# Optimization experiments

Measured on AMD Instinct MI355X. Metric: run time of the kernel, lower is better.

The kernel has to match this reference:

```python
import jax, jax.numpy as jnp
import numpy as np

B, H, E, D = 16384, 1024, 64, 128  # batch, hidden, nb_entities, wh_units==we_units


def setup_inputs() -> dict:
    key = jax.random.key(0)
    k0, k1, k2 = jax.random.split(key, 3)
    hidden_state = jax.random.normal(k0, (B, H), dtype=jnp.float32)
    # Wh: Dense(wh_units) acting on H -> D
    Wh_w = jax.random.normal(k1, (H, D), dtype=jnp.float32) * 0.02
    Wh_b = jnp.zeros((D,), dtype=jnp.float32)
    # We: nb_entities separate Dense(we_units), stacked into one [E, D, D] tensor
    We_w = jax.random.normal(k2, (E, D, D), dtype=jnp.float32) * 0.02
    We_b = jnp.zeros((E, D), dtype=jnp.float32)
    return {"hidden_state": hidden_state, "Wh_w": Wh_w, "Wh_b": Wh_b,
            "We_w": We_w, "We_b": We_b}


def reference(hidden_state, Wh_w, Wh_b, We_w, We_b):
    # reduced_dimentionality = Wh(hidden_state)            [B, D]
    r = hidden_state @ Wh_w + Wh_b
    # per-entity Dense loop + concat + transpose == one batched GEMM -> [B, E, D]
    logits = jnp.einsum('bk,ekd->bed', r, We_w) + We_b[None, :, :]
    outputs = jax.nn.softmax(logits, axis=-1)               # [B, E, D]
    # second pass: We[i] applied to outputs[:, i, :]       [B, E, D]
    vt = jnp.einsum('bek,ekd->bed', outputs, We_w) + We_b[None, :, :]
    # transpose to [B, D, E] then reduce_sum over E == sum over entity axis
    result = vt.sum(axis=1)                                 # [B, D]
    return (outputs, result)
```

## Files before the change

kernel.cpp:

```cpp
#include <hip/hip_runtime.h>
#include <hip/hip_bf16.h>

typedef __attribute__((ext_vector_type(8))) short short8;
typedef __attribute__((ext_vector_type(4))) float f32x4;
typedef __attribute__((ext_vector_type(4))) unsigned int uint4v;
typedef __attribute__((ext_vector_type(2))) unsigned int uint2v;

#define NB 16384
#define NH 1024
#define NE 64
#define ND 128
#define BR 32
#define GRP 8

static __device__ __forceinline__ unsigned short f2b(float x) {
  unsigned int u = __builtin_bit_cast(unsigned int, x);
  unsigned int r = (u + 0x7fffu + ((u >> 16) & 1u)) >> 16;
  return (unsigned short)r;
}
static __device__ __forceinline__ float b2f_lo(unsigned int u) {
  return __builtin_bit_cast(float, u << 16);
}
static __device__ __forceinline__ float b2f_hi(unsigned int u) {
  return __builtin_bit_cast(float, u & 0xffff0000u);
}

static __device__ __forceinline__ void bar_sync() {
  __builtin_amdgcn_sched_barrier(0);
  asm volatile("s_waitcnt lgkmcnt(0)" ::: "memory");
  __builtin_amdgcn_sched_barrier(0);
  __builtin_amdgcn_s_barrier();
  __builtin_amdgcn_sched_barrier(0);
}

static __device__ __forceinline__ int swz(int row, int col) {
  return (row << 7) + ((((col >> 3) ^ (row & 15)) << 3) | (col & 7));
}
static __device__ __forceinline__ int pswz(int row, int eg, int col) {
  return ((row * GRP + eg) << 7) + ((((col >> 3) ^ (row & 15)) << 3) | (col & 7));
}

__global__ __launch_bounds__(256, 1) void k0_prep(
    const float* __restrict__ Wh_w, const float* __restrict__ We_w,
    const float* __restrict__ We_b,
    unsigned short* __restrict__ WeT, unsigned short* __restrict__ WhT,
    float* __restrict__ bsum)
{
  __shared__ float tile[32][33];
  const int bid = blockIdx.x, t = threadIdx.x;
  const int i = t >> 5, j = t & 31;
  if (bid < 1024) {
    const int e = bid >> 4, tr = (bid >> 2) & 3, tc = bid & 3;
    const float* src = We_w + (size_t)e * 16384;
#pragma unroll
    for (int k = 0; k < 4; ++k)
      tile[i + 8 * k][j] = src[(size_t)(tr * 32 + i + 8 * k) * 128 + tc * 32 + j];
    __syncthreads();
    unsigned short* dst = WeT + (size_t)e * 16384;
#pragma unroll
    for (int k = 0; k < 4; ++k) {
      int row = i + 8 * k;
      dst[(size_t)(tc * 32 + row) * 128 + tr * 32 + j] = f2b(tile[j][row]);
    }
  } else if (bid < 1152) {
    const int tb = bid - 1024, tr = tb >> 2, tc = tb & 3;
#pragma unroll
    for (int k = 0; k < 4; ++k)
      tile[i + 8 * k][j] = Wh_w[(size_t)(tr * 32 + i + 8 * k) * 128 + tc * 32 + j];
    __syncthreads();
#pragma unroll
    for (int k = 0; k < 4; ++k) {
      int row = i + 8 * k;
      WhT[(size_t)(tc * 32 + row) * 1024 + tr * 32 + j] = f2b(tile[j][row]);
    }
  } else {
    if (t < 128) {
      float s = 0.f;
      for (int e = 0; e < 64; ++e) s += We_b[e * 128 + t];
      bsum[t] = s;
    }
  }
}

__global__ __launch_bounds__(256, 2) void k1_rgemm(
    const float* __restrict__ hidden, const unsigned short* __restrict__ WhT,
    const float* __restrict__ Wh_b, unsigned short* __restrict__ r_g)
{
  const int t = threadIdx.x;
  const int w = t >> 6, l = t & 63, c = l & 15, g = l >> 4;
  const int bg = w & 1, dh = w >> 1;
  const int b = blockIdx.x * 32 + 16 * bg + c;
  const float* hrow = hidden + (size_t)b * NH;
  f32x4 acc[4];
#pragma unroll
  for (int mf = 0; mf < 4; ++mf) acc[mf] = (f32x4){0.f, 0.f, 0.f, 0.f};
#pragma unroll 2
  for (int ks = 0; ks < 32; ++ks) {
    const int k0 = 8 * g + 32 * ks;
    f32x4 h0 = *(const f32x4*)(hrow + k0);
    f32x4 h1 = *(const f32x4*)(hrow + k0 + 4);
    short8 bf;
    bf[0] = (short)f2b(h0[0]); bf[1] = (short)f2b(h0[1]);
    bf[2] = (short)f2b(h0[2]); bf[3] = (short)f2b(h0[3]);
    bf[4] = (short)f2b(h1[0]); bf[5] = (short)f2b(h1[1]);
    bf[6] = (short)f2b(h1[2]); bf[7] = (short)f2b(h1[3]);
#pragma unroll
    for (int mf = 0; mf < 4; ++mf) {
      short8 af = *(const short8*)(WhT + (size_t)(64 * dh + 16 * mf + c) * NH + k0);
      acc[mf] = __builtin_amdgcn_mfma_f32_16x16x32_bf16(af, bf, acc[mf], 0, 0, 0);
    }
  }
#pragma unroll
  for (int mf = 0; mf < 4; ++mf) {
    const int d0 = 64 * dh + 16 * mf + 4 * g;
    f32x4 bias = *(const f32x4*)(Wh_b + d0);
    f32x4 v = acc[mf] + bias;
    unsigned int lo = (unsigned)f2b(v[0]) | ((unsigned)f2b(v[1]) << 16);
    unsigned int hi = (unsigned)f2b(v[2]) | ((unsigned)f2b(v[3]) << 16);
    uint2v pk = {lo, hi};
    *(uint2v*)(r_g + (size_t)b * ND + d0) = pk;
  }
}

struct SmemK2 {
  union {
    unsigned short Pst[BR * GRP * 128];
    float obuf[BR * 128];
  };
  unsigned short r_lds[BR * 128];
  float sms[4][BR];
};

static __device__ __forceinline__ void load_we_frags(
    short8 (&f)[2][4], f32x4 (&bias)[2],
    const unsigned short* __restrict__ WeT, const float* __restrict__ We_b,
    int e, int w, int c, int g)
{
  const unsigned short* base = WeT + (size_t)e * (ND * ND);
#pragma unroll
  for (int mf = 0; mf < 2; ++mf) {
    const unsigned short* rowp = base + (size_t)(16 * (2 * w + mf) + c) * ND + 8 * g;
#pragma unroll
    for (int ks = 0; ks < 4; ++ks)
      f[mf][ks] = *(const short8*)(rowp + 32 * ks);
    bias[mf] = *(const f32x4*)(We_b + e * ND + 32 * w + 16 * mf + 4 * g);
  }
}

static __device__ __forceinline__ void entity_body(
    int eg, int en, int w, int c, int g,
    short8 (&cur)[2][4], short8 (&nxt)[2][4],
    f32x4 (&bcur)[2], f32x4 (&bnxt)[2], f32x4 (&acc2)[2][2],
    const unsigned short* __restrict__ WeT, const float* __restrict__ We_b,
    SmemK2& sm)
{
  f32x4 acc1[2][2];
#pragma unroll
  for (int mf = 0; mf < 2; ++mf)
#pragma unroll
    for (int nf = 0; nf < 2; ++nf) acc1[mf][nf] = (f32x4){0.f, 0.f, 0.f, 0.f};
#pragma unroll
  for (int ks = 0; ks < 4; ++ks) {
    short8 b1[2];
#pragma unroll
    for (int nf = 0; nf < 2; ++nf)
      b1[nf] = *(const short8*)(&sm.r_lds[swz(16 * nf + c, 8 * g + 32 * ks)]);
#pragma unroll
    for (int mf = 0; mf < 2; ++mf)
#pragma unroll
      for (int nf = 0; nf < 2; ++nf)
        acc1[mf][nf] = __builtin_amdgcn_mfma_f32_16x16x32_bf16(
            cur[mf][ks], b1[nf], acc1[mf][nf], 0, 0, 0);
  }
  load_we_frags(nxt, bnxt, WeT, We_b, en, w, c, g);

#pragma unroll
  for (int mf = 0; mf < 2; ++mf)
#pragma unroll
    for (int nf = 0; nf < 2; ++nf) acc1[mf][nf] += bcur[mf];
  float s[2] = {0.f, 0.f};
#pragma unroll
  for (int nf = 0; nf < 2; ++nf) {
#pragma unroll
    for (int mf = 0; mf < 2; ++mf)
#pragma unroll
      for (int r = 0; r < 4; ++r) {
        float p = __expf(acc1[mf][nf][r]);
        acc1[mf][nf][r] = p;
        s[nf] += p;
      }
    s[nf] += __shfl_xor(s[nf], 16);
    s[nf] += __shfl_xor(s[nf], 32);
  }
  if (g == 0) {
#pragma unroll
    for (int nf = 0; nf < 2; ++nf) sm.sms[w][16 * nf + c] = s[nf];
  }
  bar_sync();
  float inv[2];
#pragma unroll
  for (int nf = 0; nf < 2; ++nf) {
    int b = 16 * nf + c;
    inv[nf] = 1.f / (sm.sms[0][b] + sm.sms[1][b] + sm.sms[2][b] + sm.sms[3][b]);
  }
#pragma unroll
  for (int mf = 0; mf < 2; ++mf)
#pragma unroll
    for (int nf = 0; nf < 2; ++nf) {
      f32x4 p = acc1[mf][nf] * inv[nf];
      unsigned int lo = (unsigned)f2b(p[0]) | ((unsigned)f2b(p[1]) << 16);
      unsigned int hi = (unsigned)f2b(p[2]) | ((unsigned)f2b(p[3]) << 16);
      uint2v pk = {lo, hi};
      *(uint2v*)(&sm.Pst[pswz(16 * nf + c, eg, 32 * w + 16 * mf + 4 * g)]) = pk;
    }
  bar_sync();

#pragma unroll
  for (int ks = 0; ks < 4; ++ks) {
    short8 a2[2];
#pragma unroll
    for (int mf2 = 0; mf2 < 2; ++mf2)
      a2[mf2] = *(const short8*)(&sm.Pst[pswz(16 * mf2 + c, eg, 8 * g + 32 * ks)]);
#pragma unroll
    for (int mf2 = 0; mf2 < 2; ++mf2)
#pragma unroll
      for (int n = 0; n < 2; ++n)
        acc2[mf2][n] = __builtin_amdgcn_mfma_f32_16x16x32_bf16(
            a2[mf2], cur[n][ks], acc2[mf2][n], 0, 0, 0);
  }
}

__global__ __launch_bounds__(256, 2) void k2_main(
    const unsigned short* __restrict__ r_g, const unsigned short* __restrict__ WeT,
    const float* __restrict__ We_b, const float* __restrict__ bsum,
    float* __restrict__ outP, float* __restrict__ outR)
{
  __shared__ SmemK2 sm;
  const int t = threadIdx.x;
  const int w = t >> 6, l = t & 63, c = l & 15, g = l >> 4;
  const int lb = (blockIdx.x & 7) * 64 + (blockIdx.x >> 3);
  const int brow0 = lb * BR;
  const int e0 = (((lb >> 6) + lb) & 7) << 3;

  for (int i = t; i < BR * 16; i += 256) {
    int row = i >> 4, ch = i & 15;
    uint4v v = *(const uint4v*)(r_g + (size_t)(brow0 + row) * ND + ch * 8);
    *(uint4v*)(&sm.r_lds[swz(row, ch * 8)]) = v;
  }
  const float bs0 = bsum[32 * w + c];
  const float bs1 = bsum[32 * w + 16 + c];

  f32x4 acc2[2][2];
#pragma unroll
  for (int i = 0; i < 2; ++i)
#pragma unroll
    for (int j = 0; j < 2; ++j) acc2[i][j] = (f32x4){0.f, 0.f, 0.f, 0.f};

  short8 wa[2][4], wb[2][4];
  f32x4 ba[2], bb[2];
  load_we_frags(wa, ba, WeT, We_b, e0, w, c, g);
  bar_sync();

#pragma unroll 1
  for (int gi = 0; gi < NE / GRP; ++gi) {
    for (int j = 0; j < GRP; j += 2) {
      const int i = gi * GRP + j;
      const int eB = (e0 + i + 1) & 63, eC = (e0 + i + 2) & 63;
      entity_body(j,     eB, w, c, g, wa, wb, ba, bb, acc2, WeT, We_b, sm);
      entity_body(j + 1, eC, w, c, g, wb, wa, bb, ba, acc2, WeT, We_b, sm);
    }
    {
      const int eg0 = (e0 + gi * GRP) & 63;
#pragma unroll
      for (int rr = 0; rr < 8; ++rr) {
        const int row = 8 * w + rr;
        float* dst = outP + ((size_t)(brow0 + row) * NE + eg0) * ND;
#pragma unroll
        for (int it = 0; it < 4; ++it) {
          const int flat = it * 256 + l * 4;
          const int eg = flat >> 7, col = flat & 127;
          uint2v u = *(const uint2v*)(&sm.Pst[pswz(row, eg, col)]);
          f32x4 v;
          v[0] = b2f_lo(u[0]); v[1] = b2f_hi(u[0]);
          v[2] = b2f_lo(u[1]); v[3] = b2f_hi(u[1]);
          __builtin_nontemporal_store(v, (f32x4*)(dst + flat));
        }
      }
    }
  }

  bar_sync();
#pragma unroll
  for (int mf2 = 0; mf2 < 2; ++mf2)
#pragma unroll
    for (int n = 0; n < 2; ++n) {
      float bs = n ? bs1 : bs0;
#pragma unroll
      for (int r = 0; r < 4; ++r)
        sm.obuf[(16 * mf2 + 4 * g + r) * ND + 32 * w + 16 * n + c] =
            acc2[mf2][n][r] + bs;
    }
  bar_sync();
  {
    const int orow = t >> 5, ocol = (t & 31) * 4;
#pragma unroll
    for (int it = 0; it < 4; ++it) {
      const int row = orow + 8 * it;
      f32x4 v = *(const f32x4*)(&sm.obuf[row * ND + ocol]);
      __builtin_nontemporal_store(
          v, (f32x4*)(outR + (size_t)(brow0 + row) * ND + ocol));
    }
  }
}

extern "C" void kernel_launch(void* const* d_in, const int* in_sizes, int n_in,
                              void* d_out, int out_size, void* d_ws, size_t ws_size,
                              hipStream_t stream)
{
  (void)in_sizes; (void)n_in; (void)out_size; (void)ws_size;
  const float* hidden = (const float*)d_in[0];
  const float* Wh_w   = (const float*)d_in[1];
  const float* Wh_b   = (const float*)d_in[2];
  const float* We_w   = (const float*)d_in[3];
  const float* We_b   = (const float*)d_in[4];
  float* outP = (float*)d_out;
  float* outR = outP + (size_t)NB * NE * ND;

  char* ws = (char*)d_ws;
  unsigned short* WeT = (unsigned short*)(ws);
  unsigned short* WhT = (unsigned short*)(ws + 2097152);
  unsigned short* r_g = (unsigned short*)(ws + 2097152 + 262144);
  float* bsum         = (float*)(ws + 2097152 + 262144 + 4194304);

  k0_prep<<<1153, 256, 0, stream>>>(Wh_w, We_w, We_b, WeT, WhT, bsum);
  k1_rgemm<<<512, 256, 0, stream>>>(hidden, WhT, Wh_b, r_g);
  k2_main<<<512, 256, 0, stream>>>(r_g, WeT, We_b, bsum, outP, outR);
}
```

Before: 248.9 us.

## Restructure entity kernel so each wave owns full softmax rows for half the entities

```diff
diff --git a/kernel.cpp b/kernel.cpp
--- a/kernel.cpp
+++ b/kernel.cpp
@@ -10,8 +10,6 @@
 #define NH 1024
 #define NE 64
 #define ND 128
-#define BR 32
-#define GRP 8
 
 static __device__ __forceinline__ unsigned short f2b(float x) {
   unsigned int u = __builtin_bit_cast(unsigned int, x);
@@ -25,26 +23,11 @@
   return __builtin_bit_cast(float, u & 0xffff0000u);
 }
 
-static __device__ __forceinline__ void bar_sync() {
-  __builtin_amdgcn_sched_barrier(0);
-  asm volatile("s_waitcnt lgkmcnt(0)" ::: "memory");
-  __builtin_amdgcn_sched_barrier(0);
-  __builtin_amdgcn_s_barrier();
-  __builtin_amdgcn_sched_barrier(0);
-}
-
-static __device__ __forceinline__ int swz(int row, int col) {
-  return (row << 7) + ((((col >> 3) ^ (row & 15)) << 3) | (col & 7));
-}
-static __device__ __forceinline__ int pswz(int row, int eg, int col) {
-  return ((row * GRP + eg) << 7) + ((((col >> 3) ^ (row & 15)) << 3) | (col & 7));
-}
-
 __global__ __launch_bounds__(256, 1) void k0_prep(
     const float* __restrict__ Wh_w, const float* __restrict__ We_w,
     const float* __restrict__ We_b,
     unsigned short* __restrict__ WeT, unsigned short* __restrict__ WhT,
-    float* __restrict__ bsum)
+    float* __restrict__ bsum, unsigned short* __restrict__ We_bb)
 {
   __shared__ float tile[32][33];
   const int bid = blockIdx.x, t = threadIdx.x;
@@ -73,12 +56,14 @@
       int row = i + 8 * k;
       WhT[(size_t)(tc * 32 + row) * 1024 + tr * 32 + j] = f2b(tile[j][row]);
     }
-  } else {
+  } else if (bid == 1152) {
     if (t < 128) {
       float s = 0.f;
       for (int e = 0; e < 64; ++e) s += We_b[e * 128 + t];
       bsum[t] = s;
     }
+  } else {
+    for (int k = t; k < NE * ND; k += 256) We_bb[k] = f2b(We_b[k]);
   }
 }
 
@@ -122,193 +107,134 @@
   }
 }
 
-struct SmemK2 {
-  union {
-    unsigned short Pst[BR * GRP * 128];
-    float obuf[BR * 128];
-  };
-  unsigned short r_lds[BR * 128];
-  float sms[4][BR];
-};
-
-static __device__ __forceinline__ void load_we_frags(
-    short8 (&f)[2][4], f32x4 (&bias)[2],
-    const unsigned short* __restrict__ WeT, const float* __restrict__ We_b,
-    int e, int w, int c, int g)
-{
-  const unsigned short* base = WeT + (size_t)e * (ND * ND);
-#pragma unroll
-  for (int mf = 0; mf < 2; ++mf) {
-    const unsigned short* rowp = base + (size_t)(16 * (2 * w + mf) + c) * ND + 8 * g;
+
+static __device__ __forceinline__ void store_slice(
+    const unsigned short* __restrict__ slice, float* __restrict__ outP,
+    int brow0, int e, int l)
+{
+#pragma unroll
+  for (int it = 0; it < 8; ++it) {
+    const int f = it * 256 + l * 4;
+    const int row = f >> 7, col = f & 127;
+    const int addr = row * 128 + ((((col >> 3) ^ row) & 15) << 3) + (col & 7);
+    uint2v u = *(const uint2v*)(slice + addr);
+    f32x4 v;
+    v[0] = b2f_lo(u[0]); v[1] = b2f_hi(u[0]);
+    v[2] = b2f_lo(u[1]); v[3] = b2f_hi(u[1]);
+    __builtin_nontemporal_store(
+        v, (f32x4*)(outP + ((size_t)(brow0 + row) * NE + e) * ND + col));
+  }
+}
+
+__global__ __launch_bounds__(128, 2) void k2_main(
+    const unsigned short* __restrict__ r_g, const unsigned short* __restrict__ WeT,
+    const unsigned short* __restrict__ We_bb, const float* __restrict__ bsum,
+    float* __restrict__ outP, float* __restrict__ outR)
+{
+  __shared__ unsigned short P_ring[2][2][16 * 128];
+  __shared__ float obuf[16 * 128];
+  const int t = threadIdx.x;
+  const int wv = t >> 6, l = t & 63, c = l & 15, g = l >> 4;
+  const int lb = (blockIdx.x & 7) * 128 + (blockIdx.x >> 3);
+  const int brow0 = lb * 16;
+  const int ebase = wv * 32;
+  const int phase = (blockIdx.x & 3) * 8;
+  unsigned short* ring = &P_ring[wv][0][0];
+
+  short8 rf[4];
+#pragma unroll
+  for (int ks = 0; ks < 4; ++ks)
+    rf[ks] = *(const short8*)(r_g + (size_t)(brow0 + c) * ND + 8 * g + 32 * ks);
+
+  f32x4 acc2[8];
+#pragma unroll
+  for (int n = 0; n < 8; ++n) acc2[n] = (f32x4){0.f, 0.f, 0.f, 0.f};
+
+#pragma unroll 1
+  for (int i = 0; i < 32; ++i) {
+    const int e = ebase + ((i + phase) & 31);
+    const unsigned short* we = WeT + (size_t)e * (ND * ND);
+    short8 f[8][4];
 #pragma unroll
     for (int ks = 0; ks < 4; ++ks)
-      f[mf][ks] = *(const short8*)(rowp + 32 * ks);
-    bias[mf] = *(const f32x4*)(We_b + e * ND + 32 * w + 16 * mf + 4 * g);
-  }
-}
-
-static __device__ __forceinline__ void entity_body(
-    int eg, int en, int w, int c, int g,
-    short8 (&cur)[2][4], short8 (&nxt)[2][4],
-    f32x4 (&bcur)[2], f32x4 (&bnxt)[2], f32x4 (&acc2)[2][2],
-    const unsigned short* __restrict__ WeT, const float* __restrict__ We_b,
-    SmemK2& sm)
-{
-  f32x4 acc1[2][2];
-#pragma unroll
-  for (int mf = 0; mf < 2; ++mf)
-#pragma unroll
-    for (int nf = 0; nf < 2; ++nf) acc1[mf][nf] = (f32x4){0.f, 0.f, 0.f, 0.f};
-#pragma unroll
-  for (int ks = 0; ks < 4; ++ks) {
-    short8 b1[2];
-#pragma unroll
-    for (int nf = 0; nf < 2; ++nf)
-      b1[nf] = *(const short8*)(&sm.r_lds[swz(16 * nf + c, 8 * g + 32 * ks)]);
-#pragma unroll
-    for (int mf = 0; mf < 2; ++mf)
-#pragma unroll
-      for (int nf = 0; nf < 2; ++nf)
-        acc1[mf][nf] = __builtin_amdgcn_mfma_f32_16x16x32_bf16(
-            cur[mf][ks], b1[nf], acc1[mf][nf], 0, 0, 0);
-  }
-  load_we_frags(nxt, bnxt, WeT, We_b, en, w, c, g);
-
-#pragma unroll
-  for (int mf = 0; mf < 2; ++mf)
-#pragma unroll
-    for (int nf = 0; nf < 2; ++nf) acc1[mf][nf] += bcur[mf];
-  float s[2] = {0.f, 0.f};
-#pragma unroll
-  for (int nf = 0; nf < 2; ++nf) {
-#pragma unroll
-    for (int mf = 0; mf < 2; ++mf)
-#pragma unroll
-      for (int r = 0; r < 4; ++r) {
-        float p = __expf(acc1[mf][nf][r]);
-        acc1[mf][nf][r] = p;
-        s[nf] += p;
-      }
-    s[nf] += __shfl_xor(s[nf], 16);
-    s[nf] += __shfl_xor(s[nf], 32);
-  }
-  if (g == 0) {
-#pragma unroll
-    for (int nf = 0; nf < 2; ++nf) sm.sms[w][16 * nf + c] = s[nf];
-  }
-  bar_sync();
-  float inv[2];
-#pragma unroll
-  for (int nf = 0; nf < 2; ++nf) {
-    int b = 16 * nf + c;
-    inv[nf] = 1.f / (sm.sms[0][b] + sm.sms[1][b] + sm.sms[2][b] + sm.sms[3][b]);
-  }
-#pragma unroll
-  for (int mf = 0; mf < 2; ++mf)
-#pragma unroll
-    for (int nf = 0; nf < 2; ++nf) {
-      f32x4 p = acc1[mf][nf] * inv[nf];
+#pragma unroll
+      for (int m = 0; m < 8; ++m)
+        f[m][ks] = *(const short8*)(we + (size_t)(16 * m + c) * ND + 8 * g + 32 * ks);
+    uint2v bb[8];
+#pragma unroll
+    for (int m = 0; m < 8; ++m)
+      bb[m] = *(const uint2v*)(We_bb + (size_t)e * ND + 16 * m + 4 * g);
+    if (i > 0) {
+      const int ep = ebase + ((i - 1 + phase) & 31);
+      store_slice(ring + ((i + 1) & 1) * 2048, outP, brow0, ep, l);
+    }
+    __builtin_amdgcn_sched_barrier(0);
+    f32x4 a1[8];
+#pragma unroll
+    for (int m = 0; m < 8; ++m) a1[m] = (f32x4){0.f, 0.f, 0.f, 0.f};
+#pragma unroll
+    for (int ks = 0; ks < 4; ++ks)
+#pragma unroll
+      for (int m = 0; m < 8; ++m)
+        a1[m] = __builtin_amdgcn_mfma_f32_16x16x32_bf16(f[m][ks], rf[ks], a1[m], 0, 0, 0);
+    float s = 0.f;
+#pragma unroll
+    for (int m = 0; m < 8; ++m) {
+      float b0 = b2f_lo(bb[m][0]), b1 = b2f_hi(bb[m][0]);
+      float b2 = b2f_lo(bb[m][1]), b3 = b2f_hi(bb[m][1]);
+      float p0 = __expf(a1[m][0] + b0); float p1 = __expf(a1[m][1] + b1);
+      float p2 = __expf(a1[m][2] + b2); float p3 = __expf(a1[m][3] + b3);
+      a1[m][0] = p0; a1[m][1] = p1; a1[m][2] = p2; a1[m][3] = p3;
+      s += (p0 + p1) + (p2 + p3);
+    }
+    s += __shfl_xor(s, 16);
+    s += __shfl_xor(s, 32);
+    const float inv = 1.f / s;
+    unsigned short* dst = ring + (i & 1) * 2048;
+#pragma unroll
+    for (int m = 0; m < 8; ++m) {
+      f32x4 p = a1[m] * inv;
       unsigned int lo = (unsigned)f2b(p[0]) | ((unsigned)f2b(p[1]) << 16);
       unsigned int hi = (unsigned)f2b(p[2]) | ((unsigned)f2b(p[3]) << 16);
       uint2v pk = {lo, hi};
-      *(uint2v*)(&sm.Pst[pswz(16 * nf + c, eg, 32 * w + 16 * mf + 4 * g)]) = pk;
-    }
-  bar_sync();
-
-#pragma unroll
-  for (int ks = 0; ks < 4; ++ks) {
-    short8 a2[2];
-#pragma unroll
-    for (int mf2 = 0; mf2 < 2; ++mf2)
-      a2[mf2] = *(const short8*)(&sm.Pst[pswz(16 * mf2 + c, eg, 8 * g + 32 * ks)]);
-#pragma unroll
-    for (int mf2 = 0; mf2 < 2; ++mf2)
-#pragma unroll
-      for (int n = 0; n < 2; ++n)
-        acc2[mf2][n] = __builtin_amdgcn_mfma_f32_16x16x32_bf16(
-            a2[mf2], cur[n][ks], acc2[mf2][n], 0, 0, 0);
-  }
-}
-
-__global__ __launch_bounds__(256, 2) void k2_main(
-    const unsigned short* __restrict__ r_g, const unsigned short* __restrict__ WeT,
-    const float* __restrict__ We_b, const float* __restrict__ bsum,
-    float* __restrict__ outP, float* __restrict__ outR)
-{
-  __shared__ SmemK2 sm;
-  const int t = threadIdx.x;
-  const int w = t >> 6, l = t & 63, c = l & 15, g = l >> 4;
-  const int lb = (blockIdx.x & 7) * 64 + (blockIdx.x >> 3);
-  const int brow0 = lb * BR;
-  const int e0 = (((lb >> 6) + lb) & 7) << 3;
-
-  for (int i = t; i < BR * 16; i += 256) {
-    int row = i >> 4, ch = i & 15;
-    uint4v v = *(const uint4v*)(r_g + (size_t)(brow0 + row) * ND + ch * 8);
-    *(uint4v*)(&sm.r_lds[swz(row, ch * 8)]) = v;
-  }
-  const float bs0 = bsum[32 * w + c];
-  const float bs1 = bsum[32 * w + 16 + c];
-
-  f32x4 acc2[2][2];
-#pragma unroll
-  for (int i = 0; i < 2; ++i)
-#pragma unroll
-    for (int j = 0; j < 2; ++j) acc2[i][j] = (f32x4){0.f, 0.f, 0.f, 0.f};
-
-  short8 wa[2][4], wb[2][4];
-  f32x4 ba[2], bb[2];
-  load_we_frags(wa, ba, WeT, We_b, e0, w, c, g);
-  bar_sync();
-
-#pragma unroll 1
-  for (int gi = 0; gi < NE / GRP; ++gi) {
-    for (int j = 0; j < GRP; j += 2) {
-      const int i = gi * GRP + j;
-      const int eB = (e0 + i + 1) & 63, eC = (e0 + i + 2) & 63;
-      entity_body(j,     eB, w, c, g, wa, wb, ba, bb, acc2, WeT, We_b, sm);
-      entity_body(j + 1, eC, w, c, g, wb, wa, bb, ba, acc2, WeT, We_b, sm);
-    }
-    {
-      const int eg0 = (e0 + gi * GRP) & 63;
-#pragma unroll
-      for (int rr = 0; rr < 8; ++rr) {
-        const int row = 8 * w + rr;
-        float* dst = outP + ((size_t)(brow0 + row) * NE + eg0) * ND;
-#pragma unroll
-        for (int it = 0; it < 4; ++it) {
-          const int flat = it * 256 + l * 4;
-          const int eg = flat >> 7, col = flat & 127;
-          uint2v u = *(const uint2v*)(&sm.Pst[pswz(row, eg, col)]);
-          f32x4 v;
-          v[0] = b2f_lo(u[0]); v[1] = b2f_hi(u[0]);
-          v[2] = b2f_lo(u[1]); v[3] = b2f_hi(u[1]);
-          __builtin_nontemporal_store(v, (f32x4*)(dst + flat));
-        }
+      const int chunk = (2 * m + (g >> 1)) ^ c;
+      *(uint2v*)(dst + c * 128 + (chunk << 3) + ((g & 1) << 2)) = pk;
+    }
+#pragma unroll
+    for (int ks2 = 0; ks2 < 4; ++ks2) {
+      short8 af = *(const short8*)(dst + c * 128 + (((g + 4 * ks2) ^ c) << 3));
+#pragma unroll
+      for (int n = 0; n < 8; ++n)
+        acc2[n] = __builtin_amdgcn_mfma_f32_16x16x32_bf16(af, f[n][ks2], acc2[n], 0, 0, 0);
+    }
+  }
+  store_slice(ring + 2048, outP, brow0, ebase + ((31 + phase) & 31), l);
+
+  if (wv == 1) {
+#pragma unroll
+    for (int n = 0; n < 8; ++n)
+#pragma unroll
+      for (int r = 0; r < 4; ++r)
+        obuf[(4 * g + r) * ND + c + 16 * n] = acc2[n][r];
+  }
+  __syncthreads();
+  if (wv == 0) {
+#pragma unroll
+    for (int n = 0; n < 8; ++n) {
+      const float bs = bsum[c + 16 * n];
+#pragma unroll
+      for (int r = 0; r < 4; ++r) {
+        const int idx = (4 * g + r) * ND + c + 16 * n;
+        obuf[idx] = acc2[n][r] + obuf[idx] + bs;
       }
     }
-  }
-
-  bar_sync();
-#pragma unroll
-  for (int mf2 = 0; mf2 < 2; ++mf2)
-#pragma unroll
-    for (int n = 0; n < 2; ++n) {
-      float bs = n ? bs1 : bs0;
-#pragma unroll
-      for (int r = 0; r < 4; ++r)
-        sm.obuf[(16 * mf2 + 4 * g + r) * ND + 32 * w + 16 * n + c] =
-            acc2[mf2][n][r] + bs;
-    }
-  bar_sync();
-  {
-    const int orow = t >> 5, ocol = (t & 31) * 4;
-#pragma unroll
-    for (int it = 0; it < 4; ++it) {
-      const int row = orow + 8 * it;
-      f32x4 v = *(const f32x4*)(&sm.obuf[row * ND + ocol]);
+#pragma unroll
+    for (int it = 0; it < 8; ++it) {
+      const int ff = it * 256 + l * 4;
+      const int row = ff >> 7, col = ff & 127;
+      f32x4 v = *(const f32x4*)(&obuf[row * ND + col]);
       __builtin_nontemporal_store(
-          v, (f32x4*)(outR + (size_t)(brow0 + row) * ND + ocol));
+          v, (f32x4*)(outR + (size_t)(brow0 + row) * ND + col));
     }
   }
 }
@@ -327,12 +253,13 @@
   float* outR = outP + (size_t)NB * NE * ND;
 
   char* ws = (char*)d_ws;
-  unsigned short* WeT = (unsigned short*)(ws);
-  unsigned short* WhT = (unsigned short*)(ws + 2097152);
-  unsigned short* r_g = (unsigned short*)(ws + 2097152 + 262144);
-  float* bsum         = (float*)(ws + 2097152 + 262144 + 4194304);
-
-  k0_prep<<<1153, 256, 0, stream>>>(Wh_w, We_w, We_b, WeT, WhT, bsum);
+  unsigned short* WeT   = (unsigned short*)(ws);
+  unsigned short* WhT   = (unsigned short*)(ws + 2097152);
+  unsigned short* r_g   = (unsigned short*)(ws + 2359296);
+  float*          bsum  = (float*)(ws + 6553600);
+  unsigned short* We_bb = (unsigned short*)(ws + 6554112);
+
+  k0_prep<<<1154, 256, 0, stream>>>(Wh_w, We_w, We_b, WeT, WhT, bsum, We_bb);
   k1_rgemm<<<512, 256, 0, stream>>>(hidden, WhT, Wh_b, r_g);
-  k2_main<<<512, 256, 0, stream>>>(r_g, WeT, We_b, bsum, outP, outR);
-}
+  k2_main<<<1024, 128, 0, stream>>>(r_g, WeT, We_bb, bsum, outP, outR);
+}
```

Result: slower. 441.1 us (+77.2%).
